# Kernel tuning notes

Hardware: AMD Instinct MI355X
Metric: run time of the kernel (lower is better)

## Reference

```python
import jax, jax.numpy as jnp
import numpy as np

N = 65536   # total nodes
E = 262144  # total edges (before self loops)
B = 2048    # graphs in batch
H = 4       # attention heads
D = 192     # per-head dim (hidden_dim // heads)
HID = 768   # hidden dim
L = 2       # num layers
EPS = 1e-5
NEG_SLOPE = 0.2  # PyG GATConv leaky_relu slope


def setup_inputs() -> dict:
    key = jax.random.key(0)
    ks = jax.random.split(key, 10)
    s = 0.02
    x = jax.random.normal(ks[0], (N, HID), dtype=jnp.float32)
    edge_index = jax.random.randint(ks[1], (2, E), 0, N)
    batch_vec = jnp.sort(jax.random.randint(ks[2], (N,), 0, B))
    W = jax.random.normal(ks[3], (L, HID, HID), dtype=jnp.float32) * s
    att_src = jax.random.normal(ks[4], (L, H, D), dtype=jnp.float32) * s
    att_dst = jax.random.normal(ks[5], (L, H, D), dtype=jnp.float32) * s
    bias = jnp.zeros((L, HID), dtype=jnp.float32)
    ln_gamma = jnp.ones((L, HID), dtype=jnp.float32)
    ln_beta = jnp.zeros((L, HID), dtype=jnp.float32)
    out_w = jax.random.normal(ks[6], (HID, HID), dtype=jnp.float32) * s
    out_b = jnp.zeros((HID,), dtype=jnp.float32)
    return dict(x=x, edge_index=edge_index, batch_vec=batch_vec, W=W,
                att_src=att_src, att_dst=att_dst, bias=bias,
                ln_gamma=ln_gamma, ln_beta=ln_beta, out_w=out_w, out_b=out_b)


def _gat_layer(x, src, dst, W_l, a_src, a_dst, b_l):
    # x: [N, HID] -> projected per-head features [N, H, D]
    xw = (x @ W_l).reshape(N, H, D)
    alpha_src = jnp.einsum('nhd,hd->nh', xw, a_src)  # [N, H]
    alpha_dst = jnp.einsum('nhd,hd->nh', xw, a_dst)  # [N, H]
    # edge attention logits (message j->i uses alpha_src[j] + alpha_dst[i])
    e = jax.nn.leaky_relu(alpha_src[src] + alpha_dst[dst], NEG_SLOPE)  # [E2, H]
    # segment softmax over incoming edges per destination node (self loops
    # guarantee every node has >= 1 incoming edge)
    m = jax.ops.segment_max(e, dst, num_segments=N)
    ex = jnp.exp(e - m[dst])
    denom = jax.ops.segment_sum(ex, dst, num_segments=N)
    alpha = ex / denom[dst]                                            # [E2, H]
    # attention-weighted scatter aggregation
    out = jax.ops.segment_sum(alpha[:, :, None] * xw[src], dst, num_segments=N)
    return out.reshape(N, HID) + b_l


def reference(x, edge_index, batch_vec, W, att_src, att_dst, bias,
              ln_gamma, ln_beta, out_w, out_b):
    loops = jnp.arange(N)
    src = jnp.concatenate([edge_index[0], loops])  # add_self_loops=True
    dst = jnp.concatenate([edge_index[1], loops])
    h = x
    for l in range(L):
        out = _gat_layer(h, src, dst, W[l], att_src[l], att_dst[l], bias[l])
        mu = jnp.mean(out, axis=-1, keepdims=True)
        var = jnp.var(out, axis=-1, keepdims=True)
        out = (out - mu) * jax.lax.rsqrt(var + EPS) * ln_gamma[l] + ln_beta[l]
        out = jax.nn.relu(out)
        h = out + h  # residual (in_dim == hidden_dim for every layer)
    # global mean pool over graphs
    ones = jnp.ones((N,), h.dtype)
    cnt = jax.ops.segment_sum(ones, batch_vec, num_segments=B)
    h_g = jax.ops.segment_sum(h, batch_vec, num_segments=B)
    h_g = h_g / jnp.maximum(cnt, 1.0)[:, None]
    return h_g @ out_w + out_b
```

## Files before the change

kernel.cpp:

```cpp
#include <hip/hip_runtime.h>
#include <hip/hip_bf16.h>

constexpr int NN  = 65536;
constexpr int EE  = 262144;
constexpr int E2  = EE + NN;
constexpr int BB  = 2048;
constexpr int HH  = 4;
constexpr int DD  = 192;
constexpr int HD  = 768;
constexpr int LL  = 2;
constexpr float EPS = 1e-5f;
constexpr float SLOPE = 0.2f;

typedef __attribute__((ext_vector_type(8))) short short8;
typedef __attribute__((ext_vector_type(4))) float f32x4;
typedef __hip_bfloat16 bf16;

__global__ void zero_k(float* __restrict__ p, int n) {
    int i = blockIdx.x * 256 + threadIdx.x;
    if (i < n) p[i] = 0.f;
}

__global__ void conv_k(const float4* __restrict__ src, bf16* __restrict__ dst, int n4) {
    int i = blockIdx.x * 256 + threadIdx.x;
    if (i >= n4) return;
    float4 v = src[i];
    bf16* o = dst + (size_t)i * 4;
    o[0] = __float2bfloat16(v.x); o[1] = __float2bfloat16(v.y);
    o[2] = __float2bfloat16(v.z); o[3] = __float2bfloat16(v.w);
}

__global__ __launch_bounds__(256) void wconv3_k(const float* __restrict__ W,
                                                const float* __restrict__ OW,
                                                bf16* __restrict__ Wt3) {
    __shared__ float tile[32][33];
    const float* src = (blockIdx.z < 2) ? (W + (size_t)blockIdx.z * HD * HD) : OW;
    bf16* dst = Wt3 + (size_t)blockIdx.z * HD * HD;
    int bx = blockIdx.x * 32;
    int by = blockIdx.y * 32;
    int tx = threadIdx.x & 31, ty = threadIdx.x >> 5;
    #pragma unroll
    for (int r = 0; r < 32; r += 8)
        tile[ty + r][tx] = src[(size_t)(by + ty + r) * HD + bx + tx];
    __syncthreads();
    #pragma unroll
    for (int r = 0; r < 32; r += 8)
        dst[(size_t)(bx + ty + r) * HD + by + tx] = __float2bfloat16(tile[tx][ty + r]);
}

__device__ __forceinline__ void load16_lds(const void* g, void* l) {
    __builtin_amdgcn_global_load_lds(
        (const __attribute__((address_space(1))) unsigned int*)g,
        (__attribute__((address_space(3))) unsigned int*)l, 16, 0, 0);
}

__global__ __launch_bounds__(512, 2) void gemm256_k(
    const bf16* __restrict__ A, const bf16* __restrict__ Bt, bf16* __restrict__ C)
{
    constexpr int K  = HD;
    constexpr int NT = K / 32;

    __shared__ __attribute__((aligned(16))) char smem[4 * 32768];

    int bid  = blockIdx.x;
    int flat = (bid & 7) * 96 + (bid >> 3);
    int by   = flat / 3;
    int bx   = flat - by * 3;
    int bm   = by * 256, bn = bx * 256;

    int tid  = threadIdx.x;
    int wid  = tid >> 6, lane = tid & 63;
    int wr   = wid >> 2, wc = wid & 3;
    int m16  = lane & 15, quad = lane >> 4;

    int prow = ((tid >> 6) << 4) | (tid & 15);
    int slot = (tid >> 4) & 3;
    const bf16* gA = A  + (size_t)(bm + prow) * K + slot * 8;
    const bf16* gB = Bt + (size_t)(bn + prow) * K + slot * 8;
    char* ldst = smem + tid * 16;

    auto STAGE = [&](int t) {
        char* d = ldst + (size_t)(t & 3) * 32768;
        const bf16* a = gA + t * 32;
        const bf16* b = gB + t * 32;
        load16_lds(a,                  d);
        load16_lds(a + (size_t)128*K,  d + 8192);
        load16_lds(b,                  d + 16384);
        load16_lds(b + (size_t)128*K,  d + 24576);
    };

    f32x4 acc[8][4];
    #pragma unroll
    for (int i = 0; i < 8; i++)
        #pragma unroll
        for (int j = 0; j < 4; j++) acc[i][j] = (f32x4)0.f;

    auto COMPUTE = [&](int t) {
        const char* ab = smem + (size_t)(t & 3) * 32768;
        const char* bb = ab + 16384;
        short8 a[8], b[4];
        #pragma unroll
        for (int n = 0; n < 4; ++n)
            b[n] = *(const short8*)(bb + (wc * 4 + n) * 1024 + lane * 16);
        #pragma unroll
        for (int m = 0; m < 8; ++m)
            a[m] = *(const short8*)(ab + (wr * 8 + m) * 1024 + lane * 16);
        __builtin_amdgcn_s_setprio(1);
        #pragma unroll
        for (int m = 0; m < 8; ++m)
            #pragma unroll
            for (int n = 0; n < 4; ++n)
                acc[m][n] = __builtin_amdgcn_mfma_f32_16x16x32_bf16(a[m], b[n], acc[m][n], 0, 0, 0);
        __builtin_amdgcn_s_setprio(0);
    };

    STAGE(0); STAGE(1); STAGE(2);
    asm volatile("s_waitcnt vmcnt(8)" ::: "memory");
    __builtin_amdgcn_s_barrier();

    for (int t = 0; t < NT - 3; ++t) {
        STAGE(t + 3);
        COMPUTE(t);
        asm volatile("s_waitcnt vmcnt(8)" ::: "memory");
        __builtin_amdgcn_s_barrier();
    }
    COMPUTE(NT - 3);
    asm volatile("s_waitcnt vmcnt(4)" ::: "memory");
    __builtin_amdgcn_s_barrier();
    COMPUTE(NT - 2);
    asm volatile("s_waitcnt vmcnt(0)" ::: "memory");
    __builtin_amdgcn_s_barrier();
    COMPUTE(NT - 1);

    #pragma unroll
    for (int m = 0; m < 8; ++m) {
        int row0 = bm + wr * 128 + m * 16 + quad * 4;
        #pragma unroll
        for (int n = 0; n < 4; ++n) {
            int col = bn + wc * 64 + n * 16 + m16;
            #pragma unroll
            for (int r = 0; r < 4; ++r)
                C[(size_t)(row0 + r) * HD + col] = __float2bfloat16(acc[m][n][r]);
        }
    }
}

template <bool BF16_OUT, bool SWIZ>
__global__ __launch_bounds__(256) void gemm_bf16_k(
    const bf16* __restrict__ A, const bf16* __restrict__ Bt,
    float* __restrict__ Cf, bf16* __restrict__ Cb, const float* __restrict__ bias)
{
    constexpr int K = HD;
    __shared__ __attribute__((aligned(16))) short As[128 * 32];
    __shared__ __attribute__((aligned(16))) short Bs[128 * 32];

    int bx, by;
    if (SWIZ) {
        int gid = blockIdx.x;
        int xcd = gid & 7, lid = gid >> 3;
        int sg = lid / 48, sl = lid - sg * 48;
        by = (xcd << 6) + (sg << 3) + (sl & 7);
        bx = sl >> 3;
    } else {
        bx = blockIdx.x; by = blockIdx.y;
    }

    int tid  = threadIdx.x;
    int wave = tid >> 6, lane = tid & 63;
    int wy = wave >> 1, wx = wave & 1;
    int m16 = lane & 15, quad = lane >> 4;
    int bm = by * 128;
    int bn = bx * 128;

    int p0 = wave * 128 + lane;
    int r0 = p0 >> 2, c0 = p0 & 3;
    int p1 = p0 + 64;
    int r1 = p1 >> 2, c1 = p1 & 3;

    const bf16* gA0 = A  + (size_t)(bm + r0) * K + c0 * 8;
    const bf16* gA1 = A  + (size_t)(bm + r1) * K + c1 * 8;
    const bf16* gB0 = Bt + (size_t)(bn + r0) * K + c0 * 8;
    const bf16* gB1 = Bt + (size_t)(bn + r1) * K + c1 * 8;

    f32x4 acc[4][4];
    #pragma unroll
    for (int i = 0; i < 4; i++)
        #pragma unroll
        for (int j = 0; j < 4; j++) acc[i][j] = (f32x4)0.f;

    const short8* Ac = (const short8*)As;
    const short8* Bc = (const short8*)Bs;

    for (int k0 = 0; k0 < K; k0 += 32) {
        load16_lds(gA0 + k0, &As[p0 * 8]);
        load16_lds(gA1 + k0, &As[p1 * 8]);
        load16_lds(gB0 + k0, &Bs[p0 * 8]);
        load16_lds(gB1 + k0, &Bs[p1 * 8]);
        __syncthreads();

        short8 a[4], b[4];
        #pragma unroll
        for (int i = 0; i < 4; i++)
            a[i] = Ac[(wy * 64 + i * 16 + m16) * 4 + quad];
        #pragma unroll
        for (int j = 0; j < 4; j++)
            b[j] = Bc[(wx * 64 + j * 16 + m16) * 4 + quad];
        #pragma unroll
        for (int i = 0; i < 4; i++)
            #pragma unroll
            for (int j = 0; j < 4; j++)
                acc[i][j] = __builtin_amdgcn_mfma_f32_16x16x32_bf16(a[i], b[j], acc[i][j], 0, 0, 0);
        __syncthreads();
    }

    #pragma unroll
    for (int j = 0; j < 4; j++) {
        int col = bn + wx * 64 + j * 16 + m16;
        float badd = (!BF16_OUT && bias) ? bias[col] : 0.f;
        #pragma unroll
        for (int i = 0; i < 4; i++) {
            int row0 = bm + wy * 64 + i * 16 + quad * 4;
            #pragma unroll
            for (int r = 0; r < 4; r++) {
                if (BF16_OUT)
                    Cb[(size_t)(row0 + r) * HD + col] = __float2bfloat16(acc[i][j][r]);
                else
                    Cf[(size_t)(row0 + r) * HD + col] = acc[i][j][r] + badd;
            }
        }
    }
}

__device__ __forceinline__ float bflo(unsigned u) { return __uint_as_float(u << 16); }
__device__ __forceinline__ float bfhi(unsigned u) { return __uint_as_float(u & 0xffff0000u); }

__global__ __launch_bounds__(256) void alpha_k(
    const bf16* __restrict__ xw,
    const float* __restrict__ asl, const float* __restrict__ adl,
    float* __restrict__ asrc, float* __restrict__ adst)
{
    int wave = threadIdx.x >> 6, lane = threadIdx.x & 63;
    int n = blockIdx.x * 4 + wave;
    int c = lane * 12;

    const bf16* row = xw + (size_t)n * HD + c;
    uint2 u0 = *(const uint2*)(row);
    uint2 u1 = *(const uint2*)(row + 4);
    uint2 u2 = *(const uint2*)(row + 8);
    float v[12] = {bflo(u0.x), bfhi(u0.x), bflo(u0.y), bfhi(u0.y),
                   bflo(u1.x), bfhi(u1.x), bflo(u1.y), bfhi(u1.y),
                   bflo(u2.x), bfhi(u2.x), bflo(u2.y), bfhi(u2.y)};

    float4 a0 = *(const float4*)(asl + c);
    float4 a1 = *(const float4*)(asl + c + 4);
    float4 a2 = *(const float4*)(asl + c + 8);
    float4 d0 = *(const float4*)(adl + c);
    float4 d1 = *(const float4*)(adl + c + 4);
    float4 d2 = *(const float4*)(adl + c + 8);
    float aa[12] = {a0.x,a0.y,a0.z,a0.w,a1.x,a1.y,a1.z,a1.w,a2.x,a2.y,a2.z,a2.w};
    float dd[12] = {d0.x,d0.y,d0.z,d0.w,d1.x,d1.y,d1.z,d1.w,d2.x,d2.y,d2.z,d2.w};

    float s1 = 0.f, s2 = 0.f;
    #pragma unroll
    for (int k = 0; k < 12; k++) { s1 += v[k] * aa[k]; s2 += v[k] * dd[k]; }

    #pragma unroll
    for (int off = 1; off < 16; off <<= 1) {
        s1 += __shfl_xor(s1, off, 64);
        s2 += __shfl_xor(s2, off, 64);
    }
    if ((lane & 15) == 0) {
        int head = lane >> 4;
        asrc[(size_t)n * HH + head] = s1;
        adst[(size_t)n * HH + head] = s2;
    }
}

__global__ void hist_k(const int* __restrict__ ei, int* __restrict__ deg) {
    int e = blockIdx.x * 256 + threadIdx.x;
    int dst = (e < EE) ? ei[EE + e] : (e - EE);
    atomicAdd(&deg[dst], 1);
}

__global__ void scan1_k(const int* __restrict__ deg, int* __restrict__ incl,
                        int* __restrict__ blocksum) {
    __shared__ int s[256];
    int t = threadIdx.x, n = blockIdx.x * 256 + t;
    int v = deg[n];
    s[t] = v;
    for (int off = 1; off < 256; off <<= 1) {
        __syncthreads();
        int tmp = (t >= off) ? s[t - off] : 0;
        __syncthreads();
        s[t] += tmp;
    }
    incl[n] = s[t];
    if (t == 255) blocksum[blockIdx.x] = s[255];
}

__global__ void scan2_k(const int* __restrict__ blocksum, int* __restrict__ blockoff) {
    __shared__ int s[256];
    int t = threadIdx.x;
    int v = blocksum[t];
    s[t] = v;
    for (int off = 1; off < 256; off <<= 1) {
        __syncthreads();
        int tmp = (t >= off) ? s[t - off] : 0;
        __syncthreads();
        s[t] += tmp;
    }
    blockoff[t] = s[t] - v;
}

__global__ void scan3_k(const int* __restrict__ deg, const int* __restrict__ blockoff,
                        int* __restrict__ incl_cursor, int* __restrict__ rowstart) {
    int t = threadIdx.x, n = blockIdx.x * 256 + t;
    int rs = blockoff[blockIdx.x] + incl_cursor[n] - deg[n];
    rowstart[n] = rs;
    incl_cursor[n] = rs;
    if (n == 0) rowstart[NN] = E2;
}

__global__ void fill_k(const int* __restrict__ ei, int* __restrict__ cursor,
                       int* __restrict__ csr_src) {
    int e = blockIdx.x * 256 + threadIdx.x;
    int src = (e < EE) ? ei[e] : (e - EE);
    int dst = (e < EE) ? ei[EE + e] : (e - EE);
    int pos = atomicAdd(&cursor[dst], 1);
    csr_src[pos] = src;
}

__global__ __launch_bounds__(256) void agg_k(
    const bf16* __restrict__ xw, const float4* __restrict__ asrc,
    const float4* __restrict__ adst, const int* __restrict__ rowstart,
    const int* __restrict__ csr_src,
    const float* __restrict__ bias_l, const float* __restrict__ gamma_l,
    const float* __restrict__ beta_l, const bf16* __restrict__ h_in,
    bf16* __restrict__ h_out)
{
    __shared__ float s_w[4][64][4];
    __shared__ int   s_src[4][64];

    int wave = threadIdx.x >> 6, lane = threadIdx.x & 63;
    int i = blockIdx.x * 4 + wave;
    int c = lane * 12;
    int myhead = lane >> 4;

    int r0 = rowstart[i], r1 = rowstart[i + 1];
    float4 ad = adst[i];

    float acc[12];
    #pragma unroll
    for (int k = 0; k < 12; k++) acc[k] = 0.f;
    float4 den = make_float4(0.f, 0.f, 0.f, 0.f);

    for (int base = r0; base < r1; base += 64) {
        int cnt = min(64, r1 - base);
        float4 w4 = make_float4(0.f, 0.f, 0.f, 0.f);
        if (lane < cnt) {
            int s = csr_src[base + lane];
            s_src[wave][lane] = s;
            float4 a = asrc[s];
            float t0 = a.x + ad.x; t0 = (t0 > 0.f) ? t0 : SLOPE * t0;
            float t1 = a.y + ad.y; t1 = (t1 > 0.f) ? t1 : SLOPE * t1;
            float t2 = a.z + ad.z; t2 = (t2 > 0.f) ? t2 : SLOPE * t2;
            float t3 = a.w + ad.w; t3 = (t3 > 0.f) ? t3 : SLOPE * t3;
            w4 = make_float4(__expf(t0), __expf(t1), __expf(t2), __expf(t3));
            *(float4*)&s_w[wave][lane][0] = w4;
        }
        den.x += w4.x; den.y += w4.y; den.z += w4.z; den.w += w4.w;
        for (int e = 0; e < cnt; e++) {
            int src = __builtin_amdgcn_readfirstlane(s_src[wave][e]);
            float wv = s_w[wave][e][myhead];
            const bf16* row = xw + (size_t)src * HD + c;
            uint2 u0 = *(const uint2*)(row);
            uint2 u1 = *(const uint2*)(row + 4);
            uint2 u2 = *(const uint2*)(row + 8);
            acc[0] += wv * bflo(u0.x); acc[1]  += wv * bfhi(u0.x);
            acc[2] += wv * bflo(u0.y); acc[3]  += wv * bfhi(u0.y);
            acc[4] += wv * bflo(u1.x); acc[5]  += wv * bfhi(u1.x);
            acc[6] += wv * bflo(u1.y); acc[7]  += wv * bfhi(u1.y);
            acc[8] += wv * bflo(u2.x); acc[9]  += wv * bfhi(u2.x);
            acc[10] += wv * bflo(u2.y); acc[11] += wv * bfhi(u2.y);
        }
    }

    #pragma unroll
    for (int off = 32; off > 0; off >>= 1) {
        den.x += __shfl_xor(den.x, off, 64);
        den.y += __shfl_xor(den.y, off, 64);
        den.z += __shfl_xor(den.z, off, 64);
        den.w += __shfl_xor(den.w, off, 64);
    }
    float deni = (myhead == 0) ? den.x : (myhead == 1) ? den.y
               : (myhead == 2) ? den.z : den.w;
    float inv = 1.f / deni;

    float4 b0 = *(const float4*)(bias_l + c);
    float4 b1 = *(const float4*)(bias_l + c + 4);
    float4 b2 = *(const float4*)(bias_l + c + 8);
    float v[12];
    v[0] = acc[0] * inv + b0.x; v[1]  = acc[1] * inv + b0.y;
    v[2] = acc[2] * inv + b0.z; v[3]  = acc[3] * inv + b0.w;
    v[4] = acc[4] * inv + b1.x; v[5]  = acc[5] * inv + b1.y;
    v[6] = acc[6] * inv + b1.z; v[7]  = acc[7] * inv + b1.w;
    v[8] = acc[8] * inv + b2.x; v[9]  = acc[9] * inv + b2.y;
    v[10] = acc[10] * inv + b2.z; v[11] = acc[11] * inv + b2.w;

    float s = 0.f;
    #pragma unroll
    for (int k = 0; k < 12; k++) s += v[k];
    #pragma unroll
    for (int off = 32; off > 0; off >>= 1) s += __shfl_xor(s, off, 64);
    float mean = s * (1.f / (float)HD);

    float q = 0.f;
    #pragma unroll
    for (int k = 0; k < 12; k++) { float d = v[k] - mean; q += d * d; }
    #pragma unroll
    for (int off = 32; off > 0; off >>= 1) q += __shfl_xor(q, off, 64);
    float rs = rsqrtf(q * (1.f / (float)HD) + EPS);

    float4 g0 = *(const float4*)(gamma_l + c);
    float4 g1 = *(const float4*)(gamma_l + c + 4);
    float4 g2 = *(const float4*)(gamma_l + c + 8);
    float4 e0 = *(const float4*)(beta_l + c);
    float4 e1 = *(const float4*)(beta_l + c + 4);
    float4 e2 = *(const float4*)(beta_l + c + 8);
    float gg[12] = {g0.x,g0.y,g0.z,g0.w,g1.x,g1.y,g1.z,g1.w,g2.x,g2.y,g2.z,g2.w};
    float bb[12] = {e0.x,e0.y,e0.z,e0.w,e1.x,e1.y,e1.z,e1.w,e2.x,e2.y,e2.z,e2.w};

    const bf16* hrow = h_in + (size_t)i * HD + c;
    uint2 hu0 = *(const uint2*)(hrow);
    uint2 hu1 = *(const uint2*)(hrow + 4);
    uint2 hu2 = *(const uint2*)(hrow + 8);
    float hres[12] = {bflo(hu0.x), bfhi(hu0.x), bflo(hu0.y), bfhi(hu0.y),
                      bflo(hu1.x), bfhi(hu1.x), bflo(hu1.y), bfhi(hu1.y),
                      bflo(hu2.x), bfhi(hu2.x), bflo(hu2.y), bfhi(hu2.y)};

    bf16 pk[12];
    #pragma unroll
    for (int k = 0; k < 12; k++) {
        float o = fmaxf((v[k] - mean) * rs * gg[k] + bb[k], 0.f) + hres[k];
        pk[k] = __float2bfloat16(o);
    }
    bf16* orow = h_out + (size_t)i * HD + c;
    *(uint2*)(orow)     = *(const uint2*)&pk[0];
    *(uint2*)(orow + 4) = *(const uint2*)&pk[4];
    *(uint2*)(orow + 8) = *(const uint2*)&pk[8];
}

__global__ __launch_bounds__(192) void pool_k(
    const bf16* __restrict__ h, const int* __restrict__ bv,
    bf16* __restrict__ hg)
{
    int g = blockIdx.x, t = threadIdx.x;
    int lo = 0, hi = NN;
    while (lo < hi) { int mid = (lo + hi) >> 1; if (bv[mid] < g) lo = mid + 1; else hi = mid; }
    int start = lo;
    hi = NN;
    while (lo < hi) { int mid = (lo + hi) >> 1; if (bv[mid] < g + 1) lo = mid + 1; else hi = mid; }
    int end = lo;
    int c = t * 4;
    float a0 = 0.f, a1 = 0.f, a2 = 0.f, a3 = 0.f;
    for (int n = start; n < end; n++) {
        uint2 u = *(const uint2*)(h + (size_t)n * HD + c);
        a0 += bflo(u.x); a1 += bfhi(u.x); a2 += bflo(u.y); a3 += bfhi(u.y);
    }
    float sc = 1.f / fmaxf((float)(end - start), 1.f);
    bf16 pk[4];
    pk[0] = __float2bfloat16(a0 * sc); pk[1] = __float2bfloat16(a1 * sc);
    pk[2] = __float2bfloat16(a2 * sc); pk[3] = __float2bfloat16(a3 * sc);
    *(uint2*)(hg + (size_t)g * HD + c) = *(const uint2*)pk;
}

extern "C" void kernel_launch(void* const* d_in, const int* in_sizes, int n_in,
                              void* d_out, int out_size, void* d_ws, size_t ws_size,
                              hipStream_t stream)
{
    (void)in_sizes; (void)n_in; (void)out_size; (void)ws_size;
    const float* x       = (const float*)d_in[0];
    const int*   ei      = (const int*)d_in[1];
    const int*   bv      = (const int*)d_in[2];
    const float* W       = (const float*)d_in[3];
    const float* att_src = (const float*)d_in[4];
    const float* att_dst = (const float*)d_in[5];
    const float* bias    = (const float*)d_in[6];
    const float* gamma   = (const float*)d_in[7];
    const float* beta    = (const float*)d_in[8];
    const float* out_w   = (const float*)d_in[9];
    const float* out_b   = (const float*)d_in[10];
    float* out = (float*)d_out;

    char* p = (char*)d_ws;
    size_t off = 0;
    auto take = [&](size_t bytes) -> char* {
        char* r = p + off;
        off = (off + bytes + 255) & ~(size_t)255;
        return r;
    };
    bf16* xw        = (bf16*)take((size_t)NN * HD * 2);
    bf16* hbf0      = (bf16*)take((size_t)NN * HD * 2);
    bf16* hbf1      = (bf16*)take((size_t)NN * HD * 2);
    bf16* Wt3       = (bf16*)take((size_t)3 * HD * HD * 2);
    float* asrc     = (float*)take((size_t)NN * HH * 4);
    float* adst     = (float*)take((size_t)NN * HH * 4);
    int*   deg      = (int*)take((size_t)NN * 4);
    int*   rowstart = (int*)take((size_t)(NN + 1) * 4);
    int*   cursor   = (int*)take((size_t)NN * 4);
    int*   blocksum = (int*)take(256 * 4);
    int*   blockoff = (int*)take(256 * 4);
    int*   csr_src  = (int*)take((size_t)E2 * 4);
    bf16*  hg       = (bf16*)take((size_t)BB * HD * 2);

    const int EB = E2 / 256;

    zero_k<<<NN / 256, 256, 0, stream>>>((float*)deg, NN);
    hist_k<<<EB, 256, 0, stream>>>(ei, deg);
    scan1_k<<<NN / 256, 256, 0, stream>>>(deg, cursor, blocksum);
    scan2_k<<<1, 256, 0, stream>>>(blocksum, blockoff);
    scan3_k<<<NN / 256, 256, 0, stream>>>(deg, blockoff, cursor, rowstart);
    fill_k<<<EB, 256, 0, stream>>>(ei, cursor, csr_src);

    conv_k<<<(NN * HD / 4 + 255) / 256, 256, 0, stream>>>((const float4*)x, hbf0, NN * HD / 4);
    wconv3_k<<<dim3(HD / 32, HD / 32, 3), 256, 0, stream>>>(W, out_w, Wt3);

    bf16* hin = hbf0;
    bf16* hout = hbf1;
    for (int l = 0; l < LL; l++) {
        gemm256_k<<<768, 512, 0, stream>>>(hin, Wt3 + (size_t)l * HD * HD, xw);
        alpha_k<<<NN / 4, 256, 0, stream>>>(xw, att_src + (size_t)l * HH * DD,
                                            att_dst + (size_t)l * HH * DD, asrc, adst);
        agg_k<<<NN / 4, 256, 0, stream>>>(xw, (const float4*)asrc, (const float4*)adst,
                                          rowstart, csr_src,
                                          bias + (size_t)l * HD, gamma + (size_t)l * HD,
                                          beta + (size_t)l * HD, hin, hout);
        bf16* tmp = hin; hin = hout; hout = tmp;
    }

    pool_k<<<BB, 192, 0, stream>>>(hin, bv, hg);
    gemm_bf16_k<false, false><<<dim3(HD / 128, BB / 128), 256, 0, stream>>>(
        hg, Wt3 + (size_t)2 * HD * HD, out, nullptr, out_b);
}
```

Baseline: 835.1 us.

## Restructure GEMM main loop into two-phase ping-pong with split staging

```diff
diff --git a/kernel.cpp b/kernel.cpp
--- a/kernel.cpp
+++ b/kernel.cpp
@@ -79,14 +79,11 @@
     const bf16* gB = Bt + (size_t)(bn + prow) * K + slot * 8;
     char* ldst = smem + tid * 16;
 
-    auto STAGE = [&](int t) {
-        char* d = ldst + (size_t)(t & 3) * 32768;
-        const bf16* a = gA + t * 32;
-        const bf16* b = gB + t * 32;
-        load16_lds(a,                  d);
-        load16_lds(a + (size_t)128*K,  d + 8192);
-        load16_lds(b,                  d + 16384);
-        load16_lds(b + (size_t)128*K,  d + 24576);
+    auto STAGE1 = [&](int t, int k) {
+        char* d = ldst + (size_t)(t & 3) * 32768 + k * 8192;
+        const bf16* s = ((k < 2) ? gA : gB) + (size_t)t * 32
+                      + ((k & 1) ? (size_t)128 * K : 0);
+        load16_lds(s, d);
     };
 
     f32x4 acc[8][4];
@@ -95,42 +92,55 @@
         #pragma unroll
         for (int j = 0; j < 4; j++) acc[i][j] = (f32x4)0.f;
 
-    auto COMPUTE = [&](int t) {
-        const char* ab = smem + (size_t)(t & 3) * 32768;
+    auto TILE2PH = [&](const char* ab, int ts) {
         const char* bb = ab + 16384;
         short8 a[8], b[4];
         #pragma unroll
-        for (int n = 0; n < 4; ++n)
-            b[n] = *(const short8*)(bb + (wc * 4 + n) * 1024 + lane * 16);
-        #pragma unroll
         for (int m = 0; m < 8; ++m)
             a[m] = *(const short8*)(ab + (wr * 8 + m) * 1024 + lane * 16);
+        b[0] = *(const short8*)(bb + (wc * 4 + 0) * 1024 + lane * 16);
+        b[1] = *(const short8*)(bb + (wc * 4 + 1) * 1024 + lane * 16);
+        if (ts >= 0) { STAGE1(ts, 0); STAGE1(ts, 1); }
+        __builtin_amdgcn_s_barrier();
+        asm volatile("s_waitcnt lgkmcnt(0)" ::: "memory");
         __builtin_amdgcn_s_setprio(1);
         #pragma unroll
-        for (int m = 0; m < 8; ++m)
-            #pragma unroll
-            for (int n = 0; n < 4; ++n)
-                acc[m][n] = __builtin_amdgcn_mfma_f32_16x16x32_bf16(a[m], b[n], acc[m][n], 0, 0, 0);
+        for (int m = 0; m < 8; ++m) {
+            acc[m][0] = __builtin_amdgcn_mfma_f32_16x16x32_bf16(a[m], b[0], acc[m][0], 0, 0, 0);
+            acc[m][1] = __builtin_amdgcn_mfma_f32_16x16x32_bf16(a[m], b[1], acc[m][1], 0, 0, 0);
+        }
         __builtin_amdgcn_s_setprio(0);
+        __builtin_amdgcn_s_barrier();
+        b[2] = *(const short8*)(bb + (wc * 4 + 2) * 1024 + lane * 16);
+        b[3] = *(const short8*)(bb + (wc * 4 + 3) * 1024 + lane * 16);
+        if (ts >= 0) { STAGE1(ts, 2); STAGE1(ts, 3); }
+        __builtin_amdgcn_s_barrier();
+        asm volatile("s_waitcnt lgkmcnt(0)" ::: "memory");
+        __builtin_amdgcn_s_setprio(1);
+        #pragma unroll
+        for (int m = 0; m < 8; ++m) {
+            acc[m][2] = __builtin_amdgcn_mfma_f32_16x16x32_bf16(a[m], b[2], acc[m][2], 0, 0, 0);
+            acc[m][3] = __builtin_amdgcn_mfma_f32_16x16x32_bf16(a[m], b[3], acc[m][3], 0, 0, 0);
+        }
+        __builtin_amdgcn_s_setprio(0);
+        if (ts >= 0) asm volatile("s_waitcnt vmcnt(4)" ::: "memory");
+        else         asm volatile("s_waitcnt vmcnt(0)" ::: "memory");
+        __builtin_amdgcn_s_barrier();
     };
 
-    STAGE(0); STAGE(1); STAGE(2);
-    asm volatile("s_waitcnt vmcnt(8)" ::: "memory");
-    __builtin_amdgcn_s_barrier();
-
-    for (int t = 0; t < NT - 3; ++t) {
-        STAGE(t + 3);
-        COMPUTE(t);
-        asm volatile("s_waitcnt vmcnt(8)" ::: "memory");
-        __builtin_amdgcn_s_barrier();
-    }
-    COMPUTE(NT - 3);
-    asm volatile("s_waitcnt vmcnt(4)" ::: "memory");
-    __builtin_amdgcn_s_barrier();
-    COMPUTE(NT - 2);
+    #pragma unroll
+    for (int k = 0; k < 4; ++k) STAGE1(0, k);
+    #pragma unroll
+    for (int k = 0; k < 4; ++k) STAGE1(1, k);
     asm volatile("s_waitcnt vmcnt(0)" ::: "memory");
     __builtin_amdgcn_s_barrier();
-    COMPUTE(NT - 1);
+
+    for (int i = 0; i < NT / 2; ++i) {
+        int t  = 2 * i;
+        int ts = (i < NT / 2 - 1) ? t + 2 : -1;
+        TILE2PH(smem + (size_t)(t & 3) * 32768,       ts);
+        TILE2PH(smem + (size_t)((t + 1) & 3) * 32768, (ts >= 0) ? ts + 1 : -1);
+    }
 
     #pragma unroll
     for (int m = 0; m < 8; ++m) {
```

Result: no change. 829.6 us (-0.7%).
